# Kernel tuning notes

Measured on AMD Instinct MI355X. Metric: run time of the kernel, lower is better.

Reference implementation:

```python
import jax, jax.numpy as jnp
import numpy as np

EPS = 1e-9
KERNEL = 3


def kernel_tile(x, kernel, stride):
    """im2col-style patch extraction. x: [B,H,W,...] -> [B,OH,OW,kernel*kernel,depth]."""
    B, H, W = x.shape[:3]
    depth = int(np.prod(x.shape[3:]))
    x = x.reshape(B, H, W, depth)
    OH = (H - kernel) // stride + 1
    OW = (W - kernel) // stride + 1
    patches = jnp.stack(
        [x[:, i:i + (OH - 1) * stride + 1:stride, j:j + (OW - 1) * stride + 1:stride, :]
         for i in range(kernel) for j in range(kernel)], axis=3)
    return patches  # [B,OH,OW,k*k,depth]


def em_routing(votes, i_act, beta_v, beta_a, routings):
    # votes: [B,S,S,I,O,16], i_act: [B,S,S,I], beta_*: [1,1,1,O]
    I, O = votes.shape[-3], votes.shape[-2]
    rr = jnp.full((I, O, 1), 1.0 / O, dtype=votes.dtype)
    i_act = i_act[..., None, None]           # [B,S,S,I,1,1]
    bv = beta_v[..., None, :, None]          # [1,1,1,1,O,1]
    ba = beta_a[..., None, :, None]
    it_min, it_max = 1.0, min(float(routings), 3.0)
    o_mean = o_act = None
    for it in range(routings):
        inv_temp = it_min + (it_max - it_min) * it / max(1.0, routings - 1.0)
        # M-step
        rr_prime = rr * i_act                                        # [B,S,S,I,O,1]
        rr_sum = jnp.sum(rr_prime, axis=-3, keepdims=True)           # [B,S,S,1,O,1]
        o_mean = jnp.sum(rr_prime * votes, axis=-3, keepdims=True) / rr_sum  # [B,S,S,1,O,16]
        o_stdv = jnp.sqrt(jnp.sum(rr_prime * jnp.square(votes - o_mean), axis=-3, keepdims=True) / rr_sum)
        o_cost = (bv + jnp.log(o_stdv + EPS)) * rr_sum               # [B,S,S,1,O,16]
        o_act = jax.nn.sigmoid(inv_temp * (ba - jnp.sum(o_cost, axis=-1, keepdims=True)))  # [B,S,S,1,O,1]
        if it < routings - 1:
            # E-step: log Gaussian prob of each vote under each output capsule
            o_p = (-jnp.sum(jnp.square(votes - o_mean) / (2.0 * jnp.square(o_stdv)), axis=-1, keepdims=True)
                   - jnp.sum(jnp.log(o_stdv + EPS), axis=-1, keepdims=True))  # [B,S,S,I,O,1]
            zz = jnp.log(o_act + EPS) + o_p
            rr = jax.nn.softmax(zz, axis=-2)                          # softmax over O
    pose = jnp.squeeze(o_mean, axis=-3)      # [B,S,S,O,16]
    act = jnp.squeeze(o_act, axis=(-3, -1))  # [B,S,S,O]
    return pose, act


def setup_inputs() -> dict:
    key = jax.random.key(0)
    ks = jax.random.split(key, 5)
    B, H, W, I_SIZE, O_SIZE = 4, 14, 14, 32, 32
    inputs_pose = jax.random.normal(ks[0], (B, H, W, I_SIZE, 4, 4), dtype=jnp.float32)
    inputs_activation = jax.random.uniform(ks[1], (B, H, W, I_SIZE), dtype=jnp.float32)
    w = jax.random.normal(ks[2], (1, 3 * 3 * I_SIZE, O_SIZE, 4, 4), dtype=jnp.float32)
    beta_v = 0.1 * jax.random.normal(ks[3], (1, 1, 1, O_SIZE), dtype=jnp.float32)
    beta_a = 0.1 * jax.random.normal(ks[4], (1, 1, 1, O_SIZE), dtype=jnp.float32)
    return {"inputs_pose": inputs_pose, "inputs_activation": inputs_activation,
            "w": w, "beta_v": beta_v, "beta_a": beta_a, "stride": 1, "routings": 3}


def reference(inputs_pose, inputs_activation, w, beta_v, beta_a, stride, routings):
    B = inputs_pose.shape[0]
    pose_size = inputs_pose.shape[-1]            # 4
    i_size = inputs_pose.shape[3]
    o_size = w.shape[2]
    tp = kernel_tile(inputs_pose, KERNEL, stride)        # [B,S,S,9,i*16]
    ta = kernel_tile(inputs_activation, KERNEL, stride)  # [B,S,S,9,i]
    S = ta.shape[1]
    I = KERNEL * KERNEL * i_size
    poses = tp.reshape(-1, I, pose_size, pose_size)      # [N,I,4,4], N = B*S*S
    acts = ta.reshape(B, S, S, I)
    # vote transform: per (input capsule, output capsule) 4x4 matmul
    votes = jnp.einsum('nipq,ioqr->niopr', poses, w[0])  # [N,I,O,4,4]
    votes = votes.reshape(B, S, S, I, o_size, pose_size * pose_size)
    pose, activation = em_routing(votes, acts, beta_v, beta_a, routings)
    pose = pose.reshape(B, S, S, o_size, pose_size, pose_size)
    return pose, activation
```

## Files before the change

### kernel.cpp

```cpp
#include <hip/hip_runtime.h>
#include <math.h>

namespace {

constexpr int SOUT = 12;
constexpr int OCAP = 32;
constexpr int PD   = 16;
constexpr int NI   = 288;
constexpr int NPOS = 4 * SOUT * SOUT;
constexpr float EPSF = 1e-9f;
constexpr size_t POSE_OUT = (size_t)NPOS * OCAP * PD;

__global__ __launch_bounds__(512, 4)
void caps_em_fused(const float* __restrict__ pose_in,
                   const float* __restrict__ act_in,
                   const float* __restrict__ wmat,
                   const float* __restrict__ beta_v,
                   const float* __restrict__ beta_a,
                   float* __restrict__ out)
{
    __shared__ __align__(16) float sP[NI * PD];
    __shared__ float sA[NI];
    __shared__ float sInv2[OCAP][PD + 1];
    __shared__ float sNeg[OCAP][PD + 1];
    __shared__ float sBias[OCAP];
    __shared__ float sRed[4][33][33];

    const int n  = blockIdx.x;
    const int b  = n / (SOUT * SOUT);
    const int yx = n % (SOUT * SOUT);
    const int y  = yx / SOUT;
    const int x  = yx % SOUT;

    const int t    = threadIdx.x;
    const int wave = t >> 6;
    const int lane = t & 63;
    const int o    = lane & 31;
    const int half = lane >> 5;

    {
        const float4* src = reinterpret_cast<const float4*>(pose_in);
        float4* dst = reinterpret_cast<float4*>(sP);
        for (int u = t; u < NI * 4; u += 512) {
            const int k = u >> 7, idx = u & 127;
            const int ki = k / 3, kj = k - ki * 3;
            const int cell = (b * 14 + y + ki) * 14 + (x + kj);
            dst[u] = src[(size_t)cell * 128 + idx];
        }
        for (int u = t; u < NI; u += 512) {
            const int k = u >> 5, c = u & 31;
            const int ki = k / 3, kj = k - ki * 3;
            const int cell = (b * 14 + y + ki) * 14 + (x + kj);
            sA[u] = act_in[(size_t)cell * 32 + c];
        }
    }
    __syncthreads();

    for (int sweep = 0; sweep < 3; ++sweep) {
        const float bias_r = (sweep > 0) ? sBias[o] : 0.f;

        float s1[PD], s2[PD];
        float s0 = 0.f;
        #pragma unroll
        for (int d = 0; d < PD; ++d) { s1[d] = 0.f; s2[d] = 0.f; }

        #pragma unroll 1
        for (int step = 0; step < NI / 16; ++step) {
            const int i = step * 16 + wave * 2 + half;

            float W[PD];
            const float* wr = wmat + ((size_t)i * OCAP + o) * PD;
            #pragma unroll
            for (int q4 = 0; q4 < 4; ++q4) {
                const float4 wv = *reinterpret_cast<const float4*>(&wr[q4 * 4]);
                W[q4*4+0] = wv.x; W[q4*4+1] = wv.y; W[q4*4+2] = wv.z; W[q4*4+3] = wv.w;
            }

            float v[PD];
            const float* pr = &sP[i * PD];
            #pragma unroll
            for (int p = 0; p < 4; ++p) {
                const float4 pv = *reinterpret_cast<const float4*>(&pr[p * 4]);
                #pragma unroll
                for (int r = 0; r < 4; ++r) {
                    float acc = pv.x * W[r];
                    acc = fmaf(pv.y, W[4  + r], acc);
                    acc = fmaf(pv.z, W[8  + r], acc);
                    acc = fmaf(pv.w, W[12 + r], acc);
                    v[p*4+r] = acc;
                }
            }

            const float a_i = sA[i];
            float rrp;
            if (sweep == 0) {
                rrp = a_i * (1.0f / 32.0f);
            } else {
                float ts = 0.f;
                #pragma unroll
                for (int d = 0; d < PD; ++d) {
                    const float h = fmaf(v[d], sInv2[o][d], sNeg[o][d]);
                    ts = fmaf(v[d], h, ts);
                }
                float zz = bias_r - ts;
                float m = zz;
                #pragma unroll
                for (int msk = 16; msk >= 1; msk >>= 1)
                    m = fmaxf(m, __shfl_xor(m, msk, 32));
                const float e = __expf(zz - m);
                float es = e;
                #pragma unroll
                for (int msk = 16; msk >= 1; msk >>= 1)
                    es += __shfl_xor(es, msk, 32);
                rrp = __fdividef(e, es) * a_i;
            }

            s0 += rrp;
            #pragma unroll
            for (int d = 0; d < PD; ++d) {
                const float rv = rrp * v[d];
                s1[d] = fmaf(rrp, v[d], s1[d]);
                s2[d] = fmaf(rv, v[d], s2[d]);
            }
        }

        #pragma unroll
        for (int d = 0; d < PD; ++d) {
            s1[d] += __shfl_xor(s1[d], 32, 64);
            s2[d] += __shfl_xor(s2[d], 32, 64);
        }
        s0 += __shfl_xor(s0, 32, 64);

        if (wave < 4 && half == 0) {
            #pragma unroll
            for (int d = 0; d < PD; ++d) {
                sRed[wave][d][o]      = s1[d];
                sRed[wave][16 + d][o] = s2[d];
            }
            sRed[wave][32][o] = s0;
        }
        __syncthreads();
        if (wave >= 4 && half == 0) {
            #pragma unroll
            for (int d = 0; d < PD; ++d) {
                sRed[wave - 4][d][o]      += s1[d];
                sRed[wave - 4][16 + d][o] += s2[d];
            }
            sRed[wave - 4][32][o] += s0;
        }
        __syncthreads();

        if (t < 256) {
            const int oo = t >> 3, dp = t & 7, d0 = dp * 2;
            float S0 = 0.f, S1a = 0.f, S1b = 0.f, S2a = 0.f, S2b = 0.f;
            #pragma unroll
            for (int r = 0; r < 4; ++r) {
                S0  += sRed[r][32][oo];
                S1a += sRed[r][d0][oo];
                S1b += sRed[r][d0 + 1][oo];
                S2a += sRed[r][16 + d0][oo];
                S2b += sRed[r][17 + d0][oo];
            }
            const float inv = 1.f / S0;
            const float m0 = S1a * inv, m1 = S1b * inv;
            const float v0 = fmaxf(fmaf(-m0, m0, S2a * inv), 0.f);
            const float v1 = fmaxf(fmaf(-m1, m1, S2b * inv), 0.f);
            if (sweep == 2) {
                float2 pv; pv.x = m0; pv.y = m1;
                *reinterpret_cast<float2*>(out + (size_t)n * (OCAP * PD) + oo * PD + d0) = pv;
            }
            const float i20 = 0.5f / fmaxf(v0, 1e-30f);
            const float i21 = 0.5f / fmaxf(v1, 1e-30f);
            float llocal = __logf(sqrtf(v0) + EPSF) + __logf(sqrtf(v1) + EPSF);
            float c0l    = m0 * m0 * i20 + m1 * m1 * i21;
            if (sweep < 2) {
                sInv2[oo][d0]     = i20;
                sInv2[oo][d0 + 1] = i21;
                sNeg[oo][d0]      = -2.f * m0 * i20;
                sNeg[oo][d0 + 1]  = -2.f * m1 * i21;
            }
            #pragma unroll
            for (int msk = 1; msk <= 4; msk <<= 1) {
                llocal += __shfl_xor(llocal, msk, 8);
                c0l    += __shfl_xor(c0l,    msk, 8);
            }
            if (dp == 0) {
                const float lt   = llocal;
                const float cost = S0 * fmaf(16.f, beta_v[oo], lt);
                const float invtemp = 1.0f + (float)sweep;
                const float oact = 1.f / (1.f + __expf(-invtemp * (beta_a[oo] - cost)));
                if (sweep < 2)
                    sBias[oo] = __logf(oact + EPSF) - lt - c0l;
                else
                    out[POSE_OUT + (size_t)n * OCAP + oo] = oact;
            }
        }
        __syncthreads();
    }
}

}

extern "C" void kernel_launch(void* const* d_in, const int* in_sizes, int n_in,
                              void* d_out, int out_size, void* d_ws, size_t ws_size,
                              hipStream_t stream) {
    const float* pose_in = (const float*)d_in[0];
    const float* act_in  = (const float*)d_in[1];
    const float* wmat    = (const float*)d_in[2];
    const float* beta_v  = (const float*)d_in[3];
    const float* beta_a  = (const float*)d_in[4];
    float* out = (float*)d_out;

    caps_em_fused<<<dim3(NPOS), dim3(512), 0, stream>>>(
        pose_in, act_in, wmat, beta_v, beta_a, out);
}
```

Measured before the change: 133.0 us.

## Halve block size, process two capsules per thread with prefetched weights

Each block now has 256 threads instead of 512, and each thread handles two input capsules per step. The weight matrices for the next pair are software-prefetched into registers while the current votes are computed. The per-sweep inverse-variance and mean terms are cached in registers. The softmax reductions use ds_swizzle instead of shuffles, and the two-stage shared-memory reduction with its extra barrier is removed. This raises per-thread ILP and cuts barriers, at the cost of higher register pressure (about 64 W registers plus accumulators) and possibly lower occupancy.

```diff
diff --git a/kernel.cpp b/kernel.cpp
--- a/kernel.cpp
+++ b/kernel.cpp
@@ -11,7 +11,30 @@
 constexpr float EPSF = 1e-9f;
 constexpr size_t POSE_OUT = (size_t)NPOS * OCAP * PD;
 
-__global__ __launch_bounds__(512, 4)
+#define SWZ(x, msk) __int_as_float(__builtin_amdgcn_ds_swizzle(__float_as_int(x), ((msk) << 10) | 0x1F))
+
+__device__ __forceinline__ void loadW(const float* __restrict__ p, float (&W)[16]) {
+    const float4 w0 = *reinterpret_cast<const float4*>(p);
+    const float4 w1 = *reinterpret_cast<const float4*>(p + 4);
+    const float4 w2 = *reinterpret_cast<const float4*>(p + 8);
+    const float4 w3 = *reinterpret_cast<const float4*>(p + 12);
+    W[0]=w0.x; W[1]=w0.y; W[2]=w0.z; W[3]=w0.w;
+    W[4]=w1.x; W[5]=w1.y; W[6]=w1.z; W[7]=w1.w;
+    W[8]=w2.x; W[9]=w2.y; W[10]=w2.z; W[11]=w2.w;
+    W[12]=w3.x; W[13]=w3.y; W[14]=w3.z; W[15]=w3.w;
+}
+
+__device__ __forceinline__ void vote16(const float* __restrict__ pr, const float (&W)[16], float (&v)[16]) {
+    #pragma unroll
+    for (int p = 0; p < 4; ++p) {
+        const float4 pv = *reinterpret_cast<const float4*>(pr + p * 4);
+        #pragma unroll
+        for (int r = 0; r < 4; ++r)
+            v[p*4+r] = fmaf(pv.x, W[r], fmaf(pv.y, W[4+r], fmaf(pv.z, W[8+r], pv.w * W[12+r])));
+    }
+}
+
+__global__ __launch_bounds__(256, 2)
 void caps_em_fused(const float* __restrict__ pose_in,
                    const float* __restrict__ act_in,
                    const float* __restrict__ wmat,
@@ -21,8 +44,8 @@
 {
     __shared__ __align__(16) float sP[NI * PD];
     __shared__ float sA[NI];
-    __shared__ float sInv2[OCAP][PD + 1];
-    __shared__ float sNeg[OCAP][PD + 1];
+    __shared__ __align__(16) float sInv2[OCAP][PD];
+    __shared__ __align__(16) float sNeg[OCAP][PD];
     __shared__ float sBias[OCAP];
     __shared__ float sRed[4][33][33];
 
@@ -34,20 +57,20 @@
 
     const int t    = threadIdx.x;
     const int wave = t >> 6;
-    const int lane = t & 63;
-    const int o    = lane & 31;
-    const int half = lane >> 5;
+    const int o    = t & 31;
+    const int woff = t >> 5;
+    const int half = woff & 1;
 
     {
         const float4* src = reinterpret_cast<const float4*>(pose_in);
         float4* dst = reinterpret_cast<float4*>(sP);
-        for (int u = t; u < NI * 4; u += 512) {
+        for (int u = t; u < NI * 4; u += 256) {
             const int k = u >> 7, idx = u & 127;
             const int ki = k / 3, kj = k - ki * 3;
             const int cell = (b * 14 + y + ki) * 14 + (x + kj);
             dst[u] = src[(size_t)cell * 128 + idx];
         }
-        for (int u = t; u < NI; u += 512) {
+        for (int u = t; u < NI; u += 256) {
             const int k = u >> 5, c = u & 31;
             const int ki = k / 3, kj = k - ki * 3;
             const int cell = (b * 14 + y + ki) * 14 + (x + kj);
@@ -56,73 +79,82 @@
     }
     __syncthreads();
 
+    const float* wbase = wmat + (size_t)(woff * 512 + o * 16);
+
+    #pragma unroll 1
     for (int sweep = 0; sweep < 3; ++sweep) {
-        const float bias_r = (sweep > 0) ? sBias[o] : 0.f;
+        float bias_r = 0.f;
+        float i2r[PD], ngr[PD];
+        if (sweep > 0) {
+            bias_r = sBias[o];
+            #pragma unroll
+            for (int d = 0; d < PD; ++d) { i2r[d] = sInv2[o][d]; ngr[d] = sNeg[o][d]; }
+        }
 
         float s1[PD], s2[PD];
         float s0 = 0.f;
         #pragma unroll
         for (int d = 0; d < PD; ++d) { s1[d] = 0.f; s2[d] = 0.f; }
 
+        float WA0[16], WB0[16], WA1[16], WB1[16];
+        loadW(wbase, WA0);
+        loadW(wbase + 4096, WB0);
+
+#define PAIR_BODY(pp, Wa, Wb, Wna, Wnb)                                          \
+        {                                                                        \
+            const int _p = (pp);                                                 \
+            if (_p < 17) {                                                       \
+                loadW(wbase + (_p + 1) * 8192, Wna);                             \
+                loadW(wbase + (_p + 1) * 8192 + 4096, Wnb);                      \
+            }                                                                    \
+            const int ia = _p * 16 + woff;                                       \
+            const int ib = ia + 8;                                               \
+            float va[16], vb[16];                                                \
+            vote16(&sP[ia * PD], Wa, va);                                        \
+            vote16(&sP[ib * PD], Wb, vb);                                        \
+            const float aa = sA[ia], ab = sA[ib];                                \
+            float rra, rrb;                                                      \
+            if (sweep == 0) {                                                    \
+                rra = aa * (1.0f / 32.0f);                                       \
+                rrb = ab * (1.0f / 32.0f);                                       \
+            } else {                                                             \
+                float tsa = 0.f, tsb = 0.f;                                      \
+                _Pragma("unroll")                                                \
+                for (int d = 0; d < PD; ++d) {                                   \
+                    tsa = fmaf(va[d], fmaf(va[d], i2r[d], ngr[d]), tsa);         \
+                    tsb = fmaf(vb[d], fmaf(vb[d], i2r[d], ngr[d]), tsb);         \
+                }                                                                \
+                const float zza = bias_r - tsa, zzb = bias_r - tsb;              \
+                float ma = zza, mb = zzb;                                        \
+                ma = fmaxf(ma, SWZ(ma, 16)); mb = fmaxf(mb, SWZ(mb, 16));        \
+                ma = fmaxf(ma, SWZ(ma, 8));  mb = fmaxf(mb, SWZ(mb, 8));         \
+                ma = fmaxf(ma, SWZ(ma, 4));  mb = fmaxf(mb, SWZ(mb, 4));         \
+                ma = fmaxf(ma, SWZ(ma, 2));  mb = fmaxf(mb, SWZ(mb, 2));         \
+                ma = fmaxf(ma, SWZ(ma, 1));  mb = fmaxf(mb, SWZ(mb, 1));         \
+                const float ea = __expf(zza - ma), eb = __expf(zzb - mb);        \
+                float sa = ea, sb = eb;                                          \
+                sa += SWZ(sa, 16); sb += SWZ(sb, 16);                            \
+                sa += SWZ(sa, 8);  sb += SWZ(sb, 8);                             \
+                sa += SWZ(sa, 4);  sb += SWZ(sb, 4);                             \
+                sa += SWZ(sa, 2);  sb += SWZ(sb, 2);                             \
+                sa += SWZ(sa, 1);  sb += SWZ(sb, 1);                             \
+                rra = __fdividef(ea, sa) * aa;                                   \
+                rrb = __fdividef(eb, sb) * ab;                                   \
+            }                                                                    \
+            s0 += rra + rrb;                                                     \
+            _Pragma("unroll")                                                    \
+            for (int d = 0; d < PD; ++d) {                                       \
+                s1[d] = fmaf(rra, va[d], fmaf(rrb, vb[d], s1[d]));               \
+                s2[d] = fmaf(rra * va[d], va[d], fmaf(rrb * vb[d], vb[d], s2[d]));\
+            }                                                                    \
+        }
+
         #pragma unroll 1
-        for (int step = 0; step < NI / 16; ++step) {
-            const int i = step * 16 + wave * 2 + half;
-
-            float W[PD];
-            const float* wr = wmat + ((size_t)i * OCAP + o) * PD;
-            #pragma unroll
-            for (int q4 = 0; q4 < 4; ++q4) {
-                const float4 wv = *reinterpret_cast<const float4*>(&wr[q4 * 4]);
-                W[q4*4+0] = wv.x; W[q4*4+1] = wv.y; W[q4*4+2] = wv.z; W[q4*4+3] = wv.w;
-            }
-
-            float v[PD];
-            const float* pr = &sP[i * PD];
-            #pragma unroll
-            for (int p = 0; p < 4; ++p) {
-                const float4 pv = *reinterpret_cast<const float4*>(&pr[p * 4]);
-                #pragma unroll
-                for (int r = 0; r < 4; ++r) {
-                    float acc = pv.x * W[r];
-                    acc = fmaf(pv.y, W[4  + r], acc);
-                    acc = fmaf(pv.z, W[8  + r], acc);
-                    acc = fmaf(pv.w, W[12 + r], acc);
-                    v[p*4+r] = acc;
-                }
-            }
-
-            const float a_i = sA[i];
-            float rrp;
-            if (sweep == 0) {
-                rrp = a_i * (1.0f / 32.0f);
-            } else {
-                float ts = 0.f;
-                #pragma unroll
-                for (int d = 0; d < PD; ++d) {
-                    const float h = fmaf(v[d], sInv2[o][d], sNeg[o][d]);
-                    ts = fmaf(v[d], h, ts);
-                }
-                float zz = bias_r - ts;
-                float m = zz;
-                #pragma unroll
-                for (int msk = 16; msk >= 1; msk >>= 1)
-                    m = fmaxf(m, __shfl_xor(m, msk, 32));
-                const float e = __expf(zz - m);
-                float es = e;
-                #pragma unroll
-                for (int msk = 16; msk >= 1; msk >>= 1)
-                    es += __shfl_xor(es, msk, 32);
-                rrp = __fdividef(e, es) * a_i;
-            }
-
-            s0 += rrp;
-            #pragma unroll
-            for (int d = 0; d < PD; ++d) {
-                const float rv = rrp * v[d];
-                s1[d] = fmaf(rrp, v[d], s1[d]);
-                s2[d] = fmaf(rv, v[d], s2[d]);
-            }
-        }
+        for (int kk = 0; kk < 9; ++kk) {
+            PAIR_BODY(2 * kk,     WA0, WB0, WA1, WB1);
+            PAIR_BODY(2 * kk + 1, WA1, WB1, WA0, WB0);
+        }
+#undef PAIR_BODY
 
         #pragma unroll
         for (int d = 0; d < PD; ++d) {
@@ -131,7 +163,7 @@
         }
         s0 += __shfl_xor(s0, 32, 64);
 
-        if (wave < 4 && half == 0) {
+        if (half == 0) {
             #pragma unroll
             for (int d = 0; d < PD; ++d) {
                 sRed[wave][d][o]      = s1[d];
@@ -140,17 +172,8 @@
             sRed[wave][32][o] = s0;
         }
         __syncthreads();
-        if (wave >= 4 && half == 0) {
-            #pragma unroll
-            for (int d = 0; d < PD; ++d) {
-                sRed[wave - 4][d][o]      += s1[d];
-                sRed[wave - 4][16 + d][o] += s2[d];
-            }
-            sRed[wave - 4][32][o] += s0;
-        }
-        __syncthreads();
-
-        if (t < 256) {
+
+        {
             const int oo = t >> 3, dp = t & 7, d0 = dp * 2;
             float S0 = 0.f, S1a = 0.f, S1b = 0.f, S2a = 0.f, S2b = 0.f;
             #pragma unroll
@@ -211,6 +234,6 @@
     const float* beta_a  = (const float*)d_in[4];
     float* out = (float*)d_out;
 
-    caps_em_fused<<<dim3(NPOS), dim3(512), 0, stream>>>(
+    caps_em_fused<<<dim3(NPOS), dim3(256), 0, stream>>>(
         pose_in, act_in, wmat, beta_v, beta_a, out);
 }
```

After: 117.9 us. 11.4% less time.
